# Kernel tuning notes

Measured on AMD Instinct MI355X. Metric: run time of the kernel, lower is better.

The kernel has to match this reference:

```python
import jax, jax.numpy as jnp
import numpy as np

N = 524288      # total trajectory tokens
D_MODEL = 256
HIDDEN = 512
OUT_DIM = 32
N_TYPES = 4


def setup_inputs() -> dict:
    key = jax.random.key(0)
    k1, k2, k3, k4 = jax.random.split(key, 4)
    x = jax.random.normal(k1, (N, D_MODEL), dtype=jnp.float32)
    types = jax.random.randint(k2, (N,), 0, N_TYPES, dtype=jnp.int64)
    W1 = jax.random.normal(k3, (N_TYPES, D_MODEL, HIDDEN), dtype=jnp.float32) / np.sqrt(D_MODEL)
    b1 = jnp.zeros((N_TYPES, HIDDEN), dtype=jnp.float32)
    W2 = jax.random.normal(k4, (N_TYPES, HIDDEN, OUT_DIM), dtype=jnp.float32) / np.sqrt(HIDDEN)
    b2 = jnp.zeros((N_TYPES, OUT_DIM), dtype=jnp.float32)
    return {"x": x, "types": types, "W1": W1, "b1": b1, "W2": W2, "b2": b2}


def reference(x, types, W1, b1, W2, b2):
    # Type-masked gather -> per-type MLP decode -> scatter back to original order.
    # The gather/argsort-scatter of the torch code is equivalent (for equal
    # per-type output dims) to computing each type's decoder and selecting the
    # rows where types == type_id; we loop over the small fixed set of types.
    n_types = W1.shape[0]
    out = jnp.zeros((x.shape[0], W2.shape[-1]), dtype=x.dtype)
    for t in range(n_types):
        h = jax.nn.relu(x @ W1[t] + b1[t])          # [N, HIDDEN]
        y = h @ W2[t] + b2[t]                        # [N, OUT_DIM]
        out = jnp.where((types == t)[:, None], y, out)
    return out
```

## Files before the change

### kernel.cpp

```cpp
#include <hip/hip_runtime.h>
#include <hip/hip_bf16.h>
#include <hip/hip_fp16.h>

#define N_TOK 524288
#define DM 256
#define HID 512
#define OUTD 32
#define NTYPE 4
#define BM 128
#define HC 64
#define NBLK 512

typedef _Float16 half8 __attribute__((ext_vector_type(8)));
typedef float f32x4 __attribute__((ext_vector_type(4)));


__global__ void count_kernel(const int* __restrict__ types, int* __restrict__ bc) {
    __shared__ int c[NTYPE];
    int tid = threadIdx.x;
    if (tid < NTYPE) c[tid] = 0;
    __syncthreads();
    int b = blockIdx.x;
    int lane = tid & 63;
    #pragma unroll
    for (int j = 0; j < 4; ++j) {
        int t = types[b * 1024 + j * 256 + tid];
        #pragma unroll
        for (int tt = 0; tt < NTYPE; ++tt) {
            unsigned long long mask = __ballot(t == tt);
            if (lane == 0) atomicAdd(&c[tt], __popcll(mask));
        }
    }
    __syncthreads();
    if (tid < NTYPE) bc[tid * NBLK + b] = c[tid];
}

__global__ void scan_blocks_kernel(const int* __restrict__ bc,
                                   int* __restrict__ bb,
                                   int* __restrict__ meta) {
    __shared__ int totals[NTYPE];
    __shared__ int typeoff[NTYPE];
    int wave = threadIdx.x >> 6, lane = threadIdx.x & 63;
    int excl[NBLK / 64];
    int running = 0;
    #pragma unroll
    for (int it = 0; it < NBLK / 64; ++it) {
        int v = bc[wave * NBLK + it * 64 + lane];
        int s = v;
        #pragma unroll
        for (int d = 1; d < 64; d <<= 1) {
            int u = __shfl_up(s, d);
            if (lane >= d) s += u;
        }
        excl[it] = running + s - v;
        running += __shfl(s, 63);
    }
    if (lane == 0) totals[wave] = running;
    __syncthreads();
    if (threadIdx.x == 0) {
        int off = 0;
        for (int tt = 0; tt < NTYPE; ++tt) {
            typeoff[tt] = off;
            meta[tt] = totals[tt];
            meta[4 + tt] = off;
            off += totals[tt];
        }
    }
    __syncthreads();
    #pragma unroll
    for (int it = 0; it < NBLK / 64; ++it)
        bb[wave * NBLK + it * 64 + lane] = typeoff[wave] + excl[it];
}

__global__ void scatter2_kernel(const int* __restrict__ types,
                                const int* __restrict__ bb,
                                int* __restrict__ idx) {
    __shared__ int base[NTYPE];
    __shared__ int wcnt[4][NTYPE];
    int b = blockIdx.x;
    int tid = threadIdx.x, wave = tid >> 6, lane = tid & 63;
    if (tid < NTYPE) base[tid] = bb[tid * NBLK + b];
    #pragma unroll
    for (int j = 0; j < 4; ++j) {
        __syncthreads();
        int i = b * 1024 + j * 256 + tid;
        int t = types[i];
        int rank = 0;
        #pragma unroll
        for (int tt = 0; tt < NTYPE; ++tt) {
            unsigned long long mask = __ballot(t == tt);
            if (t == tt) rank = __popcll(mask & ((1ull << lane) - 1ull));
            if (lane == 0) wcnt[wave][tt] = __popcll(mask);
        }
        __syncthreads();
        int pre = 0;
        for (int w = 0; w < wave; ++w) pre += wcnt[w][t];
        idx[base[t] + pre + rank] = i;
        __syncthreads();
        if (tid < NTYPE) {
            int tot = 0;
            #pragma unroll
            for (int w = 0; w < 4; ++w) tot += wcnt[w][tid];
            base[tid] += tot;
        }
    }
}


__global__ void wprep_kernel(const float* __restrict__ W1, const float* __restrict__ W2,
                             _Float16* __restrict__ W1T, _Float16* __restrict__ W2T) {
    int i = blockIdx.x * blockDim.x + threadIdx.x;
    if (i < NTYPE * HID * DM) {
        int t = i / (HID * DM);
        int r = i - t * HID * DM;
        int h = r / DM;
        int d = r - h * DM;
        W1T[i] = (_Float16)W1[(t * DM + d) * HID + h];
    }
    if (i < NTYPE * OUTD * HID) {
        int t = i / (OUTD * HID);
        int r = i - t * OUTD * HID;
        int o = r / HID;
        int h = r - o * HID;
        W2T[i] = (_Float16)W2[(t * HID + h) * OUTD + o];
    }
}


__launch_bounds__(256)
__global__ void fused_mlp_kernel(const float* __restrict__ x,
                                 const int* __restrict__ meta,
                                 const int* __restrict__ idx,
                                 const _Float16* __restrict__ W1T,
                                 const _Float16* __restrict__ W2T,
                                 const float* __restrict__ b1,
                                 const float* __restrict__ b2,
                                 float* __restrict__ out) {
    const int t = blockIdx.y;
    const int cnt = meta[t];
    const int row_base = blockIdx.x * BM;
    if (row_base >= cnt) return;
    const int off = meta[4 + t];
    const int* idx_t = idx + off;

    __shared__ __align__(16) char W1sB[HC * 512];
    __shared__ __align__(16) char HsB[BM * 128];
    __shared__ __align__(16) char W2sB[OUTD * 128];

    const int tid = threadIdx.x;
    const int wave = tid >> 6;
    const int lane = tid & 63;
    const int l15 = lane & 15;
    const int lg = lane >> 4;

    half8 afrag[2][8];
    #pragma unroll
    for (int mt = 0; mt < 2; ++mt) {
        int rl = wave * 32 + mt * 16 + l15;
        int rglob = idx_t[min(row_base + rl, cnt - 1)];
        const float* xr = x + (size_t)rglob * DM;
        #pragma unroll
        for (int kk = 0; kk < 8; ++kk) {
            int k0 = kk * 32 + lg * 8;
            float4 v0 = *(const float4*)(xr + k0);
            float4 v1 = *(const float4*)(xr + k0 + 4);
            half8 h;
            h[0] = (_Float16)v0.x; h[1] = (_Float16)v0.y;
            h[2] = (_Float16)v0.z; h[3] = (_Float16)v0.w;
            h[4] = (_Float16)v1.x; h[5] = (_Float16)v1.y;
            h[6] = (_Float16)v1.z; h[7] = (_Float16)v1.w;
            afrag[mt][kk] = h;
        }
    }

    const f32x4 fzero = {0.f, 0.f, 0.f, 0.f};
    f32x4 acc2[2][2];
    #pragma unroll
    for (int mt = 0; mt < 2; ++mt)
        #pragma unroll
        for (int nt = 0; nt < 2; ++nt)
            acc2[mt][nt] = fzero;

    const _Float16* w1t_t = W1T + (size_t)t * HID * DM;
    const _Float16* w2t_t = W2T + (size_t)t * OUTD * HID;

    for (int hc = 0; hc < HID / HC; ++hc) {
        __syncthreads();

        {
            const _Float16* src = w1t_t + hc * HC * DM;
            #pragma unroll
            for (int it = 0; it < 8; ++it) {
                int g = it * 256 + tid;
                int hr = g >> 5;
                int k0 = (g & 31) * 8;
                half8 v = *(const half8*)(src + hr * DM + k0);
                *(half8*)(W1sB + hr * 512 + ((k0 * 2) ^ ((hr & 7) << 4))) = v;
            }
        }
        {
            int orow = tid >> 3;
            int k0 = (tid & 7) * 8;
            half8 v = *(const half8*)(w2t_t + orow * HID + hc * HC + k0);
            *(half8*)(W2sB + orow * 128 + ((k0 * 2) ^ ((orow & 7) << 4))) = v;
        }
        __syncthreads();

        f32x4 acc1[2][4];
        #pragma unroll
        for (int mt = 0; mt < 2; ++mt)
            #pragma unroll
            for (int nt = 0; nt < 4; ++nt)
                acc1[mt][nt] = fzero;

        #pragma unroll
        for (int kk = 0; kk < 8; ++kk) {
            int k0 = kk * 32 + lg * 8;
            half8 bfr[4];
            #pragma unroll
            for (int nt = 0; nt < 4; ++nt) {
                int hr = nt * 16 + l15;
                bfr[nt] = *(const half8*)(W1sB + hr * 512 + ((k0 * 2) ^ ((hr & 7) << 4)));
            }
            #pragma unroll
            for (int mt = 0; mt < 2; ++mt)
                #pragma unroll
                for (int nt = 0; nt < 4; ++nt)
                    acc1[mt][nt] = __builtin_amdgcn_mfma_f32_16x16x32_f16(
                        afrag[mt][kk], bfr[nt], acc1[mt][nt], 0, 0, 0);
        }

        #pragma unroll
        for (int nt = 0; nt < 4; ++nt) {
            int col = nt * 16 + l15;
            float bias = b1[t * HID + hc * HC + col];
            #pragma unroll
            for (int mt = 0; mt < 2; ++mt) {
                #pragma unroll
                for (int j = 0; j < 4; ++j) {
                    float v = fmaxf(acc1[mt][nt][j] + bias, 0.f);
                    int r = wave * 32 + mt * 16 + lg * 4 + j;
                    *(_Float16*)(HsB + r * 128 + ((col * 2) ^ ((r & 7) << 4))) = (_Float16)v;
                }
            }
        }
        __syncthreads();

        #pragma unroll
        for (int kk = 0; kk < 2; ++kk) {
            int k0 = kk * 32 + lg * 8;
            half8 a2[2], b2f[2];
            #pragma unroll
            for (int mt = 0; mt < 2; ++mt) {
                int r = wave * 32 + mt * 16 + l15;
                a2[mt] = *(const half8*)(HsB + r * 128 + ((k0 * 2) ^ ((r & 7) << 4)));
            }
            #pragma unroll
            for (int nt = 0; nt < 2; ++nt) {
                int orow = nt * 16 + l15;
                b2f[nt] = *(const half8*)(W2sB + orow * 128 + ((k0 * 2) ^ ((orow & 7) << 4)));
            }
            #pragma unroll
            for (int mt = 0; mt < 2; ++mt)
                #pragma unroll
                for (int nt = 0; nt < 2; ++nt)
                    acc2[mt][nt] = __builtin_amdgcn_mfma_f32_16x16x32_f16(
                        a2[mt], b2f[nt], acc2[mt][nt], 0, 0, 0);
        }
    }

    const int m = min(BM, cnt - row_base);
    #pragma unroll
    for (int mt = 0; mt < 2; ++mt) {
        #pragma unroll
        for (int j = 0; j < 4; ++j) {
            int rloc = wave * 32 + mt * 16 + lg * 4 + j;
            if (rloc < m) {
                int gr = idx_t[row_base + rloc];
                #pragma unroll
                for (int nt = 0; nt < 2; ++nt) {
                    int col = nt * 16 + l15;
                    out[(size_t)gr * OUTD + col] = acc2[mt][nt][j] + b2[t * OUTD + col];
                }
            }
        }
    }
}


extern "C" void kernel_launch(void* const* d_in, const int* in_sizes, int n_in,
                              void* d_out, int out_size, void* d_ws, size_t ws_size,
                              hipStream_t stream) {
    const float* x   = (const float*)d_in[0];
    const int* types = (const int*)d_in[1];
    const float* W1  = (const float*)d_in[2];
    const float* b1  = (const float*)d_in[3];
    const float* W2  = (const float*)d_in[4];
    const float* b2  = (const float*)d_in[5];
    float* out = (float*)d_out;

    char* ws = (char*)d_ws;
    int* meta = (int*)ws;
    int* idx = (int*)(ws + 64);
    _Float16* W1T = (_Float16*)(ws + 64 + 4 * (size_t)N_TOK);
    _Float16* W2T = W1T + (size_t)NTYPE * HID * DM;
    int* bc = (int*)W1T;
    int* bb = bc + NTYPE * NBLK;

    count_kernel<<<NBLK, 256, 0, stream>>>(types, bc);
    scan_blocks_kernel<<<1, 256, 0, stream>>>(bc, bb, meta);
    scatter2_kernel<<<NBLK, 256, 0, stream>>>(types, bb, idx);
    wprep_kernel<<<(NTYPE * HID * DM) / 256, 256, 0, stream>>>(W1, W2, W1T, W2T);

    dim3 grid((N_TOK + BM - 1) / BM, NTYPE);
    fused_mlp_kernel<<<grid, 256, 0, stream>>>(x, meta, idx, W1T, W2T, b1, b2, out);
}
```

Baseline: 281.4 us.

## Double-buffer W1 chunks via direct global-to-LDS loads and per-wave hidden staging

W1 is pre-swizzled in global memory during weight prep, so each 32-wide hidden chunk can be copied straight into a double-buffered LDS slot with global_load_lds while the previous chunk is being computed. W2 fragments are now read directly from global into registers, and each wave keeps its hidden activations in a private LDS slice. That private slice removes one of the two block barriers per chunk and the W2 shared-memory staging. The chunk size is halved, so there are twice as many iterations, and the asynchronous LDS writes rely on the remaining single barrier for ordering.

```diff
diff --git a/kernel.cpp b/kernel.cpp
--- a/kernel.cpp
+++ b/kernel.cpp
@@ -8,7 +8,9 @@
 #define OUTD 32
 #define NTYPE 4
 #define BM 128
-#define HC 64
+#define HC 32
+#define NCHUNK (HID / HC)
+#define CHUNK_BYTES (HC * DM * 2)
 #define NBLK 512
 
 typedef _Float16 half8 __attribute__((ext_vector_type(8)));
@@ -112,14 +114,19 @@
     int i = blockIdx.x * blockDim.x + threadIdx.x;
     if (i < NTYPE * HID * DM) {
         int t = i / (HID * DM);
-        int r = i - t * HID * DM;
-        int h = r / DM;
-        int d = r - h * DM;
+        int r = i - t * (HID * DM);
+        int byteoff = r * 2;
+        int hc = byteoff / CHUNK_BYTES;
+        int rem = byteoff - hc * CHUNK_BYTES;
+        int hr = rem >> 9;
+        int brow = rem & 511;
+        int d = (brow ^ ((hr & 7) << 4)) >> 1;
+        int h = hc * HC + hr;
         W1T[i] = (_Float16)W1[(t * DM + d) * HID + h];
     }
     if (i < NTYPE * OUTD * HID) {
         int t = i / (OUTD * HID);
-        int r = i - t * OUTD * HID;
+        int r = i - t * (OUTD * HID);
         int o = r / HID;
         int h = r - o * HID;
         W2T[i] = (_Float16)W2[(t * HID + h) * OUTD + o];
@@ -140,12 +147,10 @@
     const int cnt = meta[t];
     const int row_base = blockIdx.x * BM;
     if (row_base >= cnt) return;
-    const int off = meta[4 + t];
-    const int* idx_t = idx + off;
-
-    __shared__ __align__(16) char W1sB[HC * 512];
-    __shared__ __align__(16) char HsB[BM * 128];
-    __shared__ __align__(16) char W2sB[OUTD * 128];
+    const int* idx_t = idx + meta[4 + t];
+
+    __shared__ __align__(16) char W1sB[2][CHUNK_BYTES];
+    __shared__ __align__(16) char HsB[4][32 * 64];
 
     const int tid = threadIdx.x;
     const int wave = tid >> 6;
@@ -181,57 +186,64 @@
         for (int nt = 0; nt < 2; ++nt)
             acc2[mt][nt] = fzero;
 
-    const _Float16* w1t_t = W1T + (size_t)t * HID * DM;
+    const char* w1base = (const char*)(W1T + (size_t)t * HID * DM);
     const _Float16* w2t_t = W2T + (size_t)t * OUTD * HID;
-
-    for (int hc = 0; hc < HID / HC; ++hc) {
-        __syncthreads();
-
-        {
-            const _Float16* src = w1t_t + hc * HC * DM;
-            #pragma unroll
-            for (int it = 0; it < 8; ++it) {
-                int g = it * 256 + tid;
-                int hr = g >> 5;
-                int k0 = (g & 31) * 8;
-                half8 v = *(const half8*)(src + hr * DM + k0);
-                *(half8*)(W1sB + hr * 512 + ((k0 * 2) ^ ((hr & 7) << 4))) = v;
+    char* myHs = HsB[wave];
+
+    #pragma unroll
+    for (int it = 0; it < 4; ++it) {
+        __builtin_amdgcn_global_load_lds(
+            (const __attribute__((address_space(1))) void*)(w1base + it * 4096 + tid * 16),
+            (__attribute__((address_space(3))) void*)(&W1sB[0][it * 4096 + tid * 16]),
+            16, 0, 0);
+    }
+    __syncthreads();
+
+    for (int hc = 0; hc < NCHUNK; ++hc) {
+        const char* cur = W1sB[hc & 1];
+
+        if (hc + 1 < NCHUNK) {
+            const char* src = w1base + (size_t)(hc + 1) * CHUNK_BYTES;
+            char* dst = W1sB[(hc + 1) & 1];
+            #pragma unroll
+            for (int it = 0; it < 4; ++it) {
+                __builtin_amdgcn_global_load_lds(
+                    (const __attribute__((address_space(1))) void*)(src + it * 4096 + tid * 16),
+                    (__attribute__((address_space(3))) void*)(dst + it * 4096 + tid * 16),
+                    16, 0, 0);
             }
         }
-        {
-            int orow = tid >> 3;
-            int k0 = (tid & 7) * 8;
-            half8 v = *(const half8*)(w2t_t + orow * HID + hc * HC + k0);
-            *(half8*)(W2sB + orow * 128 + ((k0 * 2) ^ ((orow & 7) << 4))) = v;
-        }
-        __syncthreads();
-
-        f32x4 acc1[2][4];
+
+        half8 w2f[2];
+        #pragma unroll
+        for (int nt = 0; nt < 2; ++nt)
+            w2f[nt] = *(const half8*)(w2t_t + (nt * 16 + l15) * HID + hc * HC + lg * 8);
+
+        f32x4 acc1[2][2];
         #pragma unroll
         for (int mt = 0; mt < 2; ++mt)
             #pragma unroll
-            for (int nt = 0; nt < 4; ++nt)
+            for (int nt = 0; nt < 2; ++nt)
                 acc1[mt][nt] = fzero;
 
         #pragma unroll
         for (int kk = 0; kk < 8; ++kk) {
-            int k0 = kk * 32 + lg * 8;
-            half8 bfr[4];
-            #pragma unroll
-            for (int nt = 0; nt < 4; ++nt) {
+            half8 bfr[2];
+            #pragma unroll
+            for (int nt = 0; nt < 2; ++nt) {
                 int hr = nt * 16 + l15;
-                bfr[nt] = *(const half8*)(W1sB + hr * 512 + ((k0 * 2) ^ ((hr & 7) << 4)));
+                bfr[nt] = *(const half8*)(cur + hr * 512 + ((kk * 64 + lg * 16) ^ ((hr & 7) << 4)));
             }
             #pragma unroll
             for (int mt = 0; mt < 2; ++mt)
                 #pragma unroll
-                for (int nt = 0; nt < 4; ++nt)
+                for (int nt = 0; nt < 2; ++nt)
                     acc1[mt][nt] = __builtin_amdgcn_mfma_f32_16x16x32_f16(
                         afrag[mt][kk], bfr[nt], acc1[mt][nt], 0, 0, 0);
         }
 
         #pragma unroll
-        for (int nt = 0; nt < 4; ++nt) {
+        for (int nt = 0; nt < 2; ++nt) {
             int col = nt * 16 + l15;
             float bias = b1[t * HID + hc * HC + col];
             #pragma unroll
@@ -239,34 +251,26 @@
                 #pragma unroll
                 for (int j = 0; j < 4; ++j) {
                     float v = fmaxf(acc1[mt][nt][j] + bias, 0.f);
-                    int r = wave * 32 + mt * 16 + lg * 4 + j;
-                    *(_Float16*)(HsB + r * 128 + ((col * 2) ^ ((r & 7) << 4))) = (_Float16)v;
+                    int rl = mt * 16 + lg * 4 + j;
+                    *(_Float16*)(myHs + rl * 64 + ((col * 2) ^ ((rl & 3) << 4))) = (_Float16)v;
                 }
             }
         }
+
+        half8 a2[2];
+        #pragma unroll
+        for (int mt = 0; mt < 2; ++mt) {
+            int rl = mt * 16 + l15;
+            a2[mt] = *(const half8*)(myHs + rl * 64 + ((lg * 16) ^ ((rl & 3) << 4)));
+        }
+        #pragma unroll
+        for (int mt = 0; mt < 2; ++mt)
+            #pragma unroll
+            for (int nt = 0; nt < 2; ++nt)
+                acc2[mt][nt] = __builtin_amdgcn_mfma_f32_16x16x32_f16(
+                    a2[mt], w2f[nt], acc2[mt][nt], 0, 0, 0);
+
         __syncthreads();
-
-        #pragma unroll
-        for (int kk = 0; kk < 2; ++kk) {
-            int k0 = kk * 32 + lg * 8;
-            half8 a2[2], b2f[2];
-            #pragma unroll
-            for (int mt = 0; mt < 2; ++mt) {
-                int r = wave * 32 + mt * 16 + l15;
-                a2[mt] = *(const half8*)(HsB + r * 128 + ((k0 * 2) ^ ((r & 7) << 4)));
-            }
-            #pragma unroll
-            for (int nt = 0; nt < 2; ++nt) {
-                int orow = nt * 16 + l15;
-                b2f[nt] = *(const half8*)(W2sB + orow * 128 + ((k0 * 2) ^ ((orow & 7) << 4)));
-            }
-            #pragma unroll
-            for (int mt = 0; mt < 2; ++mt)
-                #pragma unroll
-                for (int nt = 0; nt < 2; ++nt)
-                    acc2[mt][nt] = __builtin_amdgcn_mfma_f32_16x16x32_f16(
-                        a2[mt], b2f[nt], acc2[mt][nt], 0, 0, 0);
-        }
     }
 
     const int m = min(BM, cnt - row_base);
```

Result: slower. 356.5 us (+26.7%).
